# Performance work log

Hardware: AMD Instinct MI355X
Metric: run time of the kernel (lower is better)

The kernel has to match this reference:

```python
import jax, jax.numpy as jnp
import numpy as np

EPS = 1e-12  # F.normalize default eps


def setup_inputs() -> dict:
    key = jax.random.key(0)
    x = jax.random.normal(key, (10000, 512), dtype=jnp.float32)
    return {"x": x, "k": 9}


def reference(x, k):
    # F.normalize(x, p=2, dim=0): L2-normalize each feature column over points
    col_norm = jnp.sqrt(jnp.sum(x * x, axis=0, keepdims=True))  # [1, D]
    xn = x / jnp.maximum(col_norm, EPS)                          # [N, D]

    # pairwise squared euclidean distance: ||xi||^2 - 2 xi.xj + ||xj||^2
    sq = jnp.sum(xn * xn, axis=-1, keepdims=True)                # [N, 1]
    dist = sq - 2.0 * (xn @ xn.T) + sq.T                          # [N, N]

    # k nearest neighbors = top-k of negative distance
    _, nn_idx = jax.lax.top_k(-dist, k)                           # [N, k] int32

    n = x.shape[0]
    center_idx = jnp.broadcast_to(jnp.arange(n, dtype=nn_idx.dtype)[:, None], (n, k))
    edge_idx = jnp.stack((nn_idx, center_idx), axis=0)            # [2, N, k]
    return edge_idx
```

## Files before the change

kernel.cpp:

```cpp
#include <hip/hip_runtime.h>
#include <math.h>

#define DD 512
#define NBLKA 400

#define PM 128
#define PN 128
#define KB 64
#define CSPLIT 6
#define NC 12
#define PBUF 32
#define PBSTRIDE (PBUF + 4)
#define NCTOT (CSPLIT*NC)
#define KOUTMAX 16
#define RS_MARGIN 2e-4f

typedef __attribute__((ext_vector_type(8))) short bf16x8;
typedef __attribute__((ext_vector_type(4))) float f32x4;

static __device__ __forceinline__ unsigned short f2bf(float f) {
    unsigned u = __float_as_uint(f);
    u += 0x7fff + ((u >> 16) & 1);
    return (unsigned short)(u >> 16);
}

__global__ void colsum_partial(const float* __restrict__ x, double* __restrict__ partial,
                               int N, int rows_per_block) {
    int b = blockIdx.x;
    int t = threadIdx.x;
    int r0 = b * rows_per_block;
    int r1 = min(r0 + rows_per_block, N);
    double s0 = 0.0, s1 = 0.0;
    for (int r = r0; r < r1; ++r) {
        float v0 = x[(size_t)r * DD + t];
        float v1 = x[(size_t)r * DD + t + 256];
        s0 += (double)v0 * (double)v0;
        s1 += (double)v1 * (double)v1;
    }
    partial[(size_t)b * DD + t]       = s0;
    partial[(size_t)b * DD + t + 256] = s1;
}

__global__ void colnorm_finish(const double* __restrict__ partial, double* __restrict__ rn,
                               double* __restrict__ w, int nblk) {
    int c = threadIdx.x;
    double s = 0.0;
    for (int b = 0; b < nblk; ++b) s += partial[(size_t)b * DD + c];
    double n = fmax(sqrt(s), 1e-12);
    double r = 1.0 / n;
    rn[c]  = r;
    w[c]   = r * r;
}

__global__ void row_sq(const float* __restrict__ x, const double* __restrict__ rn,
                       double* __restrict__ sq, float* __restrict__ sqf,
                       unsigned short* __restrict__ xnbf, int N) {
    int i = blockIdx.x;
    int t = threadIdx.x;
    double a0 = (double)x[(size_t)i * DD + t]       * rn[t];
    double a1 = (double)x[(size_t)i * DD + t + 256] * rn[t + 256];
    xnbf[(size_t)i * DD + t]       = f2bf((float)a0);
    xnbf[(size_t)i * DD + t + 256] = f2bf((float)a1);
    double local = a0 * a0 + a1 * a1;
    __shared__ double red[256];
    red[t] = local;
    __syncthreads();
    for (int off = 128; off > 0; off >>= 1) {
        if (t < off) red[t] += red[t + off];
        __syncthreads();
    }
    if (t == 0) { sq[i] = red[0]; sqf[i] = (float)red[0]; }
}

__global__ __launch_bounds__(256, 2) void gemm_prefilter(
    const unsigned short* __restrict__ xnbf,
    const float* __restrict__ sqf, int* __restrict__ cand, float* __restrict__ cands,
    int N, int ntileM, int ntileN)
{
    __shared__ unsigned short A_s[2][PM][32];
    __shared__ unsigned short B_s[2][PN][32];
    __shared__ __align__(16) float Bsc[PM][PBSTRIDE];
    __shared__ __align__(16) int   Bid[PM][PBSTRIDE];
    __shared__ float sqi_s[PM];
    __shared__ float sqj_s[PN];
    __shared__ float thr_s[PM];
    __shared__ int   cnt_s[PM];
    __shared__ int   flag_s;

    const int bid   = blockIdx.x;
    const int q     = bid & 7;
    const int s     = bid >> 3;
    const int ridx  = s / CSPLIT;
    const int split = s - ridx * CSPLIT;
    const int rowb  = q + 8 * ridx;
    if (rowb >= ntileM) return;
    const int row0  = rowb * PM;

    const int t      = threadIdx.x;
    const int lane15 = t & 15;
    const int quad   = (t >> 4) & 3;
    const int wave   = t >> 6;
    const int wr     = (wave >> 1) * 64;
    const int wc     = (wave & 1) * 64;

    if (t == 0) flag_s = 0;
    if (t < PM) {
        int i = row0 + t;
        sqi_s[t] = (i < N) ? sqf[i] : 0.f;
        thr_s[t] = __builtin_inff();
        cnt_s[t] = 0;
    }

    float ls[NC];
    int   li[NC];
#pragma unroll
    for (int m = 0; m < NC; ++m) { ls[m] = __builtin_inff(); li[m] = 0x7fffffff; }

    f32x4 acc[4][4];

    for (int tile = split; tile < ntileN; tile += CSPLIT) {
        int col0 = tile * PN;

        if (t < PN) {
            int j = col0 + t;
            sqj_s[t] = (j < N) ? sqf[j] : __builtin_inff();
        }
#pragma unroll
        for (int mt = 0; mt < 4; ++mt)
#pragma unroll
            for (int nt = 0; nt < 4; ++nt)
                acc[mt][nt] = (f32x4){0.f, 0.f, 0.f, 0.f};

#pragma unroll 1
        for (int kc = 0; kc < DD; kc += KB) {
#pragma unroll
            for (int l = 0; l < 4; ++l) {
                int e    = t + l * 256;
                int half = e >> 9;
                int re   = e & 511;
                int row  = re >> 2;
                int c    = re & 3;
                size_t gA = (size_t)(row0 + row) * DD + kc + half * 32 + c * 8;
                __builtin_amdgcn_global_load_lds(
                    (const unsigned int*)(xnbf + gA),
                    (unsigned int*)((unsigned short*)A_s + (size_t)e * 8), 16, 0, 0);
                size_t gB = (size_t)(col0 + row) * DD + kc + half * 32 + c * 8;
                __builtin_amdgcn_global_load_lds(
                    (const unsigned int*)(xnbf + gB),
                    (unsigned int*)((unsigned short*)B_s + (size_t)e * 8), 16, 0, 0);
            }
            __syncthreads();
#pragma unroll
            for (int ks = 0; ks < 2; ++ks) {
                bf16x8 af[4], bfg[4];
#pragma unroll
                for (int mt = 0; mt < 4; ++mt)
                    af[mt] = *(const bf16x8*)&A_s[ks][wr + mt * 16 + lane15][quad * 8];
#pragma unroll
                for (int nt = 0; nt < 4; ++nt)
                    bfg[nt] = *(const bf16x8*)&B_s[ks][wc + nt * 16 + lane15][quad * 8];
#pragma unroll
                for (int mt = 0; mt < 4; ++mt)
#pragma unroll
                    for (int nt = 0; nt < 4; ++nt)
                        acc[mt][nt] = __builtin_amdgcn_mfma_f32_16x16x32_bf16(
                            af[mt], bfg[nt], acc[mt][nt], 0, 0, 0);
            }
            __syncthreads();
        }
#pragma unroll
        for (int mt = 0; mt < 4; ++mt)
#pragma unroll
            for (int nt = 0; nt < 4; ++nt)
#pragma unroll
                for (int reg = 0; reg < 4; ++reg) {
                    int rl = wr + mt * 16 + quad * 4 + reg;
                    int cl = wc + nt * 16 + lane15;
                    float g = acc[mt][nt][reg];
                    acc[mt][nt][reg] = (sqi_s[rl] - 2.f * g) + sqj_s[cl];
                }

        bool tile_edge = (col0 + PN > N);
        unsigned long long done = 0ull;
        for (;;) {
#pragma unroll
            for (int mt = 0; mt < 4; ++mt)
#pragma unroll
                for (int reg = 0; reg < 4; ++reg) {
                    const unsigned long long gb =
                        (0x1111ull << reg) << (mt * 16);
                    int rl = wr + mt * 16 + quad * 4 + reg;
                    float th = thr_s[rl];
                    float gmin = fminf(fminf(acc[mt][0][reg], acc[mt][1][reg]),
                                       fminf(acc[mt][2][reg], acc[mt][3][reg]));
                    if (!tile_edge && gmin > th) { done |= gb; continue; }
                    if ((done & gb) == gb) continue;
#pragma unroll
                    for (int nt = 0; nt < 4; ++nt) {
                        const unsigned long long bit = 1ull << (mt * 16 + nt * 4 + reg);
                        if (!(done & bit)) {
                            float sv = acc[mt][nt][reg];
                            int   j  = col0 + wc + nt * 16 + lane15;
                            if (j < N && sv <= th) {
                                int pos = atomicAdd(&cnt_s[rl], 1);
                                if (pos < PBUF) {
                                    Bsc[rl][pos] = sv;
                                    Bid[rl][pos] = j;
                                    done |= bit;
                                }
                            } else {
                                done |= bit;
                            }
                        }
                    }
                }
            if (done != ~0ull) flag_s = 1;
            __syncthreads();
            if (t < PM) {
                int c = cnt_s[t];
                if (c > PBUF) c = PBUF;
                cnt_s[t] = 0;
                for (int m0 = 0; m0 < c; m0 += 4) {
                    float4 s4 = *(const float4*)&Bsc[t][m0];
                    int4   j4 = *(const int4*)&Bid[t][m0];
#pragma unroll
                    for (int e = 0; e < 4; ++e) {
                        if (m0 + e >= c) break;
                        float sv = (e == 0) ? s4.x : (e == 1) ? s4.y : (e == 2) ? s4.z : s4.w;
                        int   j  = (e == 0) ? j4.x : (e == 1) ? j4.y : (e == 2) ? j4.z : j4.w;
                        if (sv < ls[NC - 1] || (sv == ls[NC - 1] && j < li[NC - 1])) {
                            float cs = sv; int cj = j;
#pragma unroll
                            for (int p = 0; p < NC; ++p) {
                                bool lt = (cs < ls[p]) || (cs == ls[p] && cj < li[p]);
                                float ts = ls[p]; int tj = li[p];
                                if (lt) { ls[p] = cs; li[p] = cj; cs = ts; cj = tj; }
                            }
                        }
                    }
                }
                thr_s[t] = ls[NC - 1];
            }
            __syncthreads();
            int go = flag_s;
            __syncthreads();
            if (t == 0) flag_s = 0;
            __syncthreads();
            if (!go) break;
        }
    }
    if (t < PM) {
        int i = row0 + t;
        if (i < N) {
#pragma unroll
            for (int m = 0; m < NC; ++m) {
                cand [(size_t)i * NCTOT + split * NC + m] = li[m];
                cands[(size_t)i * NCTOT + split * NC + m] = ls[m];
            }
        }
    }
}

__global__ __launch_bounds__(256) void rescore_topk(
    const float* __restrict__ x, const double* __restrict__ w,
    const double* __restrict__ sq, const int* __restrict__ cand,
    const float* __restrict__ cands, int* __restrict__ out, int N, int k)
{
    __shared__ float Ssc[4][NCTOT];
    int lane = threadIdx.x & 63;
    int wid  = threadIdx.x >> 6;
    int i = blockIdx.x * 4 + wid;
    if (i >= N) return;

    size_t base = (size_t)i * NCTOT;
    Ssc[wid][lane] = cands[base + lane];
    if (lane < NCTOT - 64) Ssc[wid][64 + lane] = cands[base + 64 + lane];

    float p0 = Ssc[wid][lane];
    float p1 = Ssc[wid][64 + (lane & 7)];
    int c0 = 0, c1 = 0;
    for (int m = 0; m < NCTOT; ++m) {
        float s = Ssc[wid][m];
        c0 += (s <= p0); c1 += (s <= p1);
    }
    float best = __builtin_inff();
    if (c0 >= k) best = p0;
    if (c1 >= k && p1 < best) best = p1;
#pragma unroll
    for (int off = 32; off > 0; off >>= 1)
        best = fminf(best, __shfl_xor(best, off, 64));
    float cut = best + RS_MARGIN;

    double aw[8];
#pragma unroll
    for (int c = 0; c < 8; ++c) {
        int d = lane + 64 * c;
        aw[c] = (double)x[(size_t)i * DD + d] * w[d];
    }
    double sqi = sq[i];

    double bs[KOUTMAX];
    int    bj[KOUTMAX];
    for (int r = 0; r < k; ++r) { bs[r] = __builtin_inf(); bj[r] = 0x7fffffff; }

    int pend = -1;
    for (int m = 0; m <= NCTOT; ++m) {
        int j1cand = -1;
        if (m < NCTOT) {
            if (Ssc[wid][m] > cut) continue;
            j1cand = cand[base + m];
            if (pend < 0) { pend = j1cand; continue; }
        } else if (pend < 0) {
            break;
        }
        int j0 = pend, j1 = j1cand;
        pend = -1;
        const float* q0 = &x[(size_t)j0 * DD + lane];
        const float* q1 = (j1 >= 0) ? &x[(size_t)j1 * DD + lane] : q0;
        float v0[8], v1[8];
#pragma unroll
        for (int c = 0; c < 8; ++c) v0[c] = q0[64 * c];
#pragma unroll
        for (int c = 0; c < 8; ++c) v1[c] = q1[64 * c];
        double d0 = 0.0, d1 = 0.0;
#pragma unroll
        for (int c = 0; c < 8; ++c) d0 = fma(aw[c], (double)v0[c], d0);
#pragma unroll
        for (int c = 0; c < 8; ++c) d1 = fma(aw[c], (double)v1[c], d1);
#pragma unroll
        for (int off = 32; off > 0; off >>= 1) {
            d0 += __shfl_xor(d0, off, 64);
            d1 += __shfl_xor(d1, off, 64);
        }
        double s0 = (sqi - 2.0 * d0) + sq[j0];
        double s1 = (j1 >= 0) ? (sqi - 2.0 * d1) + sq[j1] : __builtin_inf();
#pragma unroll 1
        for (int pick = 0; pick < 2; ++pick) {
            double sv = pick ? s1 : s0;
            int    j  = pick ? j1 : j0;
            if (j < 0) continue;
            if (sv < bs[k - 1] || (sv == bs[k - 1] && j < bj[k - 1])) {
                int pos = k - 1;
                while (pos > 0) {
                    double ps = bs[pos - 1]; int pj = bj[pos - 1];
                    if (!(sv < ps || (sv == ps && j < pj))) break;
                    bs[pos] = ps; bj[pos] = pj;
                    --pos;
                }
                bs[pos] = sv; bj[pos] = j;
            }
        }
    }
    if (lane == 0) {
        for (int r = 0; r < k; ++r) {
            out[(size_t)i * k + r]                 = bj[r];
            out[(size_t)N * k + (size_t)i * k + r] = i;
        }
    }
}

extern "C" void kernel_launch(void* const* d_in, const int* in_sizes, int n_in,
                              void* d_out, int out_size, void* d_ws, size_t ws_size,
                              hipStream_t stream) {
    const float* x = (const float*)d_in[0];
    int N = in_sizes[0] / DD;
    int k = out_size / (2 * N);
    if (k > KOUTMAX) k = KOUTMAX;

    char* ws = (char*)d_ws;
    double*         partial = (double*)ws;
    double*         rn      = (double*)(ws + 1638400);
    double*         w       = (double*)(ws + 1642496);
    double*         sq      = (double*)(ws + 1646592);
    float*          sqf     = (float*) (ws + 1726592);
    unsigned short* xnbf    = (unsigned short*)(ws + 1766592);
    int*            cand    = (int*)   (ws + 12006592);
    float*          cands   = (float*) (ws + 14886592);

    int rpb = (N + NBLKA - 1) / NBLKA;
    hipLaunchKernelGGL(colsum_partial, dim3(NBLKA), dim3(256), 0, stream, x, partial, N, rpb);
    hipLaunchKernelGGL(colnorm_finish, dim3(1), dim3(512), 0, stream, partial, rn, w, NBLKA);
    hipLaunchKernelGGL(row_sq, dim3(N), dim3(256), 0, stream, x, rn, sq, sqf, xnbf, N);

    int ntileM = (N + PM - 1) / PM;
    int ntileN = (N + PN - 1) / PN;
    int rows_per_xcd = (ntileM + 7) / 8;
    int nblk = 8 * rows_per_xcd * CSPLIT;
    hipLaunchKernelGGL(gemm_prefilter, dim3(nblk), dim3(256), 0, stream,
                       xnbf, sqf, cand, cands, N, ntileM, ntileN);

    hipLaunchKernelGGL(rescore_topk, dim3((N + 3) / 4), dim3(256), 0, stream,
                       x, w, sq, cand, cands, (int*)d_out, N, k);
}
```

Before: 785.8 us.

## Alias candidate buffers onto GEMM tiles, raise occupancy and column split

The per-row candidate buffers now reuse the A/B shared-memory tile storage instead of separate arrays, which cuts LDS use so four blocks can fit per CU. An extra barrier protects the aliased buffers. The column split doubles to 12, giving more blocks and a larger candidate set for rescore_topk to scan, which now uses three pivots per lane. Buffer slots are XOR-swizzled to avoid LDS bank conflicts. The risks are register pressure under the tighter launch bound, the added sync, and more rescoring work.

```diff
diff --git a/kernel.cpp b/kernel.cpp
--- a/kernel.cpp
+++ b/kernel.cpp
@@ -7,10 +7,10 @@
 #define PM 128
 #define PN 128
 #define KB 64
-#define CSPLIT 6
+#define CSPLIT 12
 #define NC 12
-#define PBUF 32
-#define PBSTRIDE (PBUF + 4)
+#define PBUF 28
+#define PBSTRIDE 32
 #define NCTOT (CSPLIT*NC)
 #define KOUTMAX 16
 #define RS_MARGIN 2e-4f
@@ -72,20 +72,21 @@
     if (t == 0) { sq[i] = red[0]; sqf[i] = (float)red[0]; }
 }
 
-__global__ __launch_bounds__(256, 2) void gemm_prefilter(
+__global__ __launch_bounds__(256, 4) void gemm_prefilter(
     const unsigned short* __restrict__ xnbf,
     const float* __restrict__ sqf, int* __restrict__ cand, float* __restrict__ cands,
     int N, int ntileM, int ntileN)
 {
-    __shared__ unsigned short A_s[2][PM][32];
-    __shared__ unsigned short B_s[2][PN][32];
-    __shared__ __align__(16) float Bsc[PM][PBSTRIDE];
-    __shared__ __align__(16) int   Bid[PM][PBSTRIDE];
+    __shared__ __align__(16) unsigned short A_s[2][PM][32];
+    __shared__ __align__(16) unsigned short B_s[2][PN][32];
     __shared__ float sqi_s[PM];
     __shared__ float sqj_s[PN];
     __shared__ float thr_s[PM];
     __shared__ int   cnt_s[PM];
     __shared__ int   flag_s;
+
+    float (*Bsc)[PBSTRIDE] = (float (*)[PBSTRIDE]) &A_s[0][0][0];
+    int   (*Bid)[PBSTRIDE] = (int   (*)[PBSTRIDE]) &B_s[0][0][0];
 
     const int bid   = blockIdx.x;
     const int q     = bid & 7;
@@ -125,6 +126,7 @@
             int j = col0 + t;
             sqj_s[t] = (j < N) ? sqf[j] : __builtin_inff();
         }
+        __syncthreads();
 #pragma unroll
         for (int mt = 0; mt < 4; ++mt)
 #pragma unroll
@@ -204,8 +206,9 @@
                             if (j < N && sv <= th) {
                                 int pos = atomicAdd(&cnt_s[rl], 1);
                                 if (pos < PBUF) {
-                                    Bsc[rl][pos] = sv;
-                                    Bid[rl][pos] = j;
+                                    int e = (((pos >> 2) ^ (rl & 7)) << 2) | (pos & 3);
+                                    Bsc[rl][e] = sv;
+                                    Bid[rl][e] = j;
                                     done |= bit;
                                 }
                             } else {
@@ -221,8 +224,9 @@
                 if (c > PBUF) c = PBUF;
                 cnt_s[t] = 0;
                 for (int m0 = 0; m0 < c; m0 += 4) {
-                    float4 s4 = *(const float4*)&Bsc[t][m0];
-                    int4   j4 = *(const int4*)&Bid[t][m0];
+                    int g = ((m0 >> 2) ^ (t & 7)) << 2;
+                    float4 s4 = *(const float4*)&Bsc[t][g];
+                    int4   j4 = *(const int4*)&Bid[t][g];
 #pragma unroll
                     for (int e = 0; e < 4; ++e) {
                         if (m0 + e >= c) break;
@@ -273,19 +277,22 @@
     if (i >= N) return;
 
     size_t base = (size_t)i * NCTOT;
-    Ssc[wid][lane] = cands[base + lane];
-    if (lane < NCTOT - 64) Ssc[wid][64 + lane] = cands[base + 64 + lane];
+    Ssc[wid][lane]      = cands[base + lane];
+    Ssc[wid][64 + lane] = cands[base + 64 + lane];
+    if (lane < NCTOT - 128) Ssc[wid][128 + lane] = cands[base + 128 + lane];
 
     float p0 = Ssc[wid][lane];
-    float p1 = Ssc[wid][64 + (lane & 7)];
-    int c0 = 0, c1 = 0;
+    float p1 = Ssc[wid][64 + lane];
+    float p2 = Ssc[wid][128 + (lane & 15)];
+    int c0 = 0, c1 = 0, c2 = 0;
     for (int m = 0; m < NCTOT; ++m) {
         float s = Ssc[wid][m];
-        c0 += (s <= p0); c1 += (s <= p1);
+        c0 += (s <= p0); c1 += (s <= p1); c2 += (s <= p2);
     }
     float best = __builtin_inff();
     if (c0 >= k) best = p0;
     if (c1 >= k && p1 < best) best = p1;
+    if (c2 >= k && p2 < best) best = p2;
 #pragma unroll
     for (int off = 32; off > 0; off >>= 1)
         best = fminf(best, __shfl_xor(best, off, 64));
@@ -375,7 +382,7 @@
     float*          sqf     = (float*) (ws + 1726592);
     unsigned short* xnbf    = (unsigned short*)(ws + 1766592);
     int*            cand    = (int*)   (ws + 12006592);
-    float*          cands   = (float*) (ws + 14886592);
+    float*          cands   = (float*) (ws + 17766592);
 
     int rpb = (N + NBLKA - 1) / NBLKA;
     hipLaunchKernelGGL(colsum_partial, dim3(NBLKA), dim3(256), 0, stream, x, partial, N, rpb);
```

After: 1.035 ms. 1.32x slower.

## Double-buffer GEMM K-loop with async global-to-LDS prefetch and aliased LDS

Applied to the files above, without the earlier changes.

Restructures the GEMM main loop so the next K chunk is loaded directly into a second LDS buffer while MFMAs consume the current one, using explicit vmcnt waits and raw barriers. A and B staging buffers now share one raw LDS block with the score/index scratch arrays to keep total LDS usage similar. This aims to hide global memory latency behind matrix math, at the cost of more delicate synchronisation and aliasing between the GEMM buffers and the selection scratch.

```diff
diff --git a/kernel.cpp b/kernel.cpp
--- a/kernel.cpp
+++ b/kernel.cpp
@@ -10,7 +10,7 @@
 #define CSPLIT 6
 #define NC 12
 #define PBUF 32
-#define PBSTRIDE (PBUF + 4)
+#define PBSTRIDE 36
 #define NCTOT (CSPLIT*NC)
 #define KOUTMAX 16
 #define RS_MARGIN 2e-4f
@@ -77,15 +77,15 @@
     const float* __restrict__ sqf, int* __restrict__ cand, float* __restrict__ cands,
     int N, int ntileM, int ntileN)
 {
-    __shared__ unsigned short A_s[2][PM][32];
-    __shared__ unsigned short B_s[2][PN][32];
-    __shared__ __align__(16) float Bsc[PM][PBSTRIDE];
-    __shared__ __align__(16) int   Bid[PM][PBSTRIDE];
+    __shared__ __align__(16) unsigned char lds_raw[65536];
     __shared__ float sqi_s[PM];
     __shared__ float sqj_s[PN];
     __shared__ float thr_s[PM];
     __shared__ int   cnt_s[PM];
     __shared__ int   flag_s;
+
+    float (*Bsc)[PBSTRIDE] = (float (*)[PBSTRIDE]) lds_raw;
+    int   (*Bid)[PBSTRIDE] = (int   (*)[PBSTRIDE]) (lds_raw + 32768);
 
     const int bid   = blockIdx.x;
     const int q     = bid & 7;
@@ -125,14 +125,15 @@
             int j = col0 + t;
             sqj_s[t] = (j < N) ? sqf[j] : __builtin_inff();
         }
+        __syncthreads();
+
 #pragma unroll
         for (int mt = 0; mt < 4; ++mt)
 #pragma unroll
             for (int nt = 0; nt < 4; ++nt)
                 acc[mt][nt] = (f32x4){0.f, 0.f, 0.f, 0.f};
 
-#pragma unroll 1
-        for (int kc = 0; kc < DD; kc += KB) {
+        auto STAGE = [&](int kc, int buf) {
 #pragma unroll
             for (int l = 0; l < 4; ++l) {
                 int e    = t + l * 256;
@@ -143,22 +144,41 @@
                 size_t gA = (size_t)(row0 + row) * DD + kc + half * 32 + c * 8;
                 __builtin_amdgcn_global_load_lds(
                     (const unsigned int*)(xnbf + gA),
-                    (unsigned int*)((unsigned short*)A_s + (size_t)e * 8), 16, 0, 0);
+                    (unsigned int*)(lds_raw + (size_t)buf * 16384 + (size_t)e * 16), 16, 0, 0);
                 size_t gB = (size_t)(col0 + row) * DD + kc + half * 32 + c * 8;
                 __builtin_amdgcn_global_load_lds(
                     (const unsigned int*)(xnbf + gB),
-                    (unsigned int*)((unsigned short*)B_s + (size_t)e * 8), 16, 0, 0);
-            }
-            __syncthreads();
+                    (unsigned int*)(lds_raw + 32768 + (size_t)buf * 16384 + (size_t)e * 16), 16, 0, 0);
+            }
+        };
+
+        STAGE(0, 0);
+#pragma unroll 1
+        for (int cc = 0; cc < 8; ++cc) {
+            if (cc < 7) {
+                STAGE((cc + 1) * KB, (cc + 1) & 1);
+                __builtin_amdgcn_sched_barrier(0);
+                asm volatile("s_waitcnt vmcnt(8)" ::: "memory");
+            } else {
+                __builtin_amdgcn_sched_barrier(0);
+                asm volatile("s_waitcnt vmcnt(0)" ::: "memory");
+            }
+            __builtin_amdgcn_s_barrier();
+            __builtin_amdgcn_sched_barrier(0);
+
+            const unsigned short (*Ab)[PM][32] =
+                (const unsigned short (*)[PM][32])(lds_raw + (size_t)(cc & 1) * 16384);
+            const unsigned short (*Bb)[PN][32] =
+                (const unsigned short (*)[PN][32])(lds_raw + 32768 + (size_t)(cc & 1) * 16384);
 #pragma unroll
             for (int ks = 0; ks < 2; ++ks) {
                 bf16x8 af[4], bfg[4];
 #pragma unroll
                 for (int mt = 0; mt < 4; ++mt)
-                    af[mt] = *(const bf16x8*)&A_s[ks][wr + mt * 16 + lane15][quad * 8];
+                    af[mt] = *(const bf16x8*)&Ab[ks][wr + mt * 16 + lane15][quad * 8];
 #pragma unroll
                 for (int nt = 0; nt < 4; ++nt)
-                    bfg[nt] = *(const bf16x8*)&B_s[ks][wc + nt * 16 + lane15][quad * 8];
+                    bfg[nt] = *(const bf16x8*)&Bb[ks][wc + nt * 16 + lane15][quad * 8];
 #pragma unroll
                 for (int mt = 0; mt < 4; ++mt)
 #pragma unroll
@@ -166,8 +186,10 @@
                         acc[mt][nt] = __builtin_amdgcn_mfma_f32_16x16x32_bf16(
                             af[mt], bfg[nt], acc[mt][nt], 0, 0, 0);
             }
-            __syncthreads();
-        }
+            __builtin_amdgcn_sched_barrier(0);
+            __builtin_amdgcn_s_barrier();
+        }
+
 #pragma unroll
         for (int mt = 0; mt < 4; ++mt)
 #pragma unroll
```

Measured after the change: 774.0 us. Within noise of the previous version (-1.5%).
